# Performance work log

Hardware: AMD Instinct MI355X
Metric: run time of the kernel (lower is better)

## Reference

```python
import jax, jax.numpy as jnp
import numpy as np


def _tanh_approx(x):
    return x * jax.lax.rsqrt(1.0 + x * x)


def _lru(u, nu_log, gamma_log, Bm, Cm, Dv):
    # u: [B,T,H]; nu_log/gamma_log: [N]; Bm: [N,H]; Cm: [H,N]; Dv: [H]
    A = jnp.exp(-jnp.exp(nu_log))                       # [N], |A|<1
    Bu = jnp.exp(gamma_log) * jnp.einsum('bth,nh->btn', u, Bm)  # [B,T,N]
    A_full = jnp.broadcast_to(A, Bu.shape)
    # diagonal linear recurrence h_t = A*h_{t-1} + Bu_t via parallel scan
    def comb(c1, c2):
        a1, b1 = c1
        a2, b2 = c2
        return (a1 * a2, a2 * b1 + b2)
    _, h = jax.lax.associative_scan(comb, (A_full, Bu), axis=1)  # inclusive scan
    # module uses the state delayed by one step (out[0]=0, out[t]=h_{t-1})
    h_prev = jnp.pad(h[:, :-1, :], ((0, 0), (1, 0), (0, 0)))
    y = jnp.einsum('btn,hn->bth', h_prev, Cm) + Dv * u
    return y


def _model_block(x, nu_log, gamma_log, Bm, Cm, Dv, Wlin, blin):
    y = _lru(x, nu_log, gamma_log, Bm, Cm, Dv)
    y = _tanh_approx(y) @ Wlin.T + blin
    return y + x


def setup_inputs() -> dict:
    key = jax.random.key(0)
    ks = jax.random.split(key, 10)
    B_, T_, N, H, D = 16, 65536, 64, 64, 4
    r_min, r_max = 0.8, 1.0
    u = jax.random.uniform(ks[0], (D, N))
    nu_log = jnp.log(-0.5 * jnp.log(u * (r_max ** 2 - r_min ** 2) + r_min ** 2))
    A = jnp.exp(-jnp.exp(nu_log))
    gamma_log = jnp.log(jnp.sqrt(1.0 - A ** 2))
    Bm = jax.random.normal(ks[1], (D, N, H)) / np.sqrt(2.0 * H)
    Cm = jax.random.normal(ks[2], (D, H, N)) / np.sqrt(N)
    Dv = jax.random.normal(ks[3], (D, H))
    Wlin = jax.random.normal(ks[4], (D, H, H)) / np.sqrt(H)
    blin = jnp.zeros((D, H))
    Win = jax.random.normal(ks[5], (H, 1))
    Wout = jax.random.normal(ks[6], (1, H)) / np.sqrt(H)
    x = jax.random.normal(ks[7], (B_, T_, 1))
    return {"x": x, "Win": Win, "nu_log": nu_log, "gamma_log": gamma_log,
            "Bm": Bm, "Cm": Cm, "Dv": Dv, "Wlin": Wlin, "blin": blin, "Wout": Wout}


def reference(x, Win, nu_log, gamma_log, Bm, Cm, Dv, Wlin, blin, Wout):
    h = x @ Win.T  # [B,T,H]
    depth = nu_log.shape[0]
    for i in range(depth):
        h = _model_block(h, nu_log[i], gamma_log[i], Bm[i], Cm[i], Dv[i], Wlin[i], blin[i])
    return h @ Wout.T  # [B,T,1]
```

## Files before the change

### kernel.cpp

```cpp
#include <hip/hip_runtime.h>

#define B_ 16
#define T_ 65536
#define H_ 64
#define DEPTH_ 4
#define CHUNK 128
#define NCH (T_ / CHUNK)

typedef _Float16 f16;
typedef f16 f16x8 __attribute__((ext_vector_type(8)));
typedef float f32x4 __attribute__((ext_vector_type(4)));
typedef unsigned u32x4 __attribute__((ext_vector_type(4)));

#define MFMA(a, b, c) __builtin_amdgcn_mfma_f32_16x16x32_f16(a, b, c, 0, 0, 0)
#define SWZ(t, k) ((t) * 64 + ((k) ^ (((t) & 7) << 2)))

union U4F8 { u32x4 u; f16x8 h; };

__device__ __forceinline__ f16x8 ldfrag(const f16* p) { return *(const f16x8*)p; }

__global__ __launch_bounds__(256)
void prep(const float* __restrict__ Win, const float* __restrict__ nu,
          const float* __restrict__ ga, const float* __restrict__ Bm,
          const float* __restrict__ Cm, const float* __restrict__ Dv,
          const float* __restrict__ Wl,
          f16* __restrict__ BmH, f16* __restrict__ BmL,
          f16* __restrict__ CmH, f16* __restrict__ CmL,
          f16* __restrict__ WlH, float* __restrict__ atab, float* __restrict__ sc)
{
    const int tid = threadIdx.x;
    for (int l = 0; l < DEPTH_; ++l) {
        for (int idx = tid; idx < 4096; idx += 256) {
            int n = idx >> 6;
            float g = expf(ga[l * 64 + n]);
            float v = Bm[l * 4096 + idx] * g;
            f16 h = (f16)v;
            BmH[l * 4096 + idx] = h;
            BmL[l * 4096 + idx] = (f16)(v - (float)h);
            float cv = Cm[l * 4096 + idx];
            h = (f16)cv;
            CmH[l * 4096 + idx] = h;
            CmL[l * 4096 + idx] = (f16)(cv - (float)h);
            WlH[l * 4096 + idx] = (f16)Wl[l * 4096 + idx];
        }
        if (tid < 64) {
            int n = tid;
            float ex = expf(nu[l * 64 + n]);
            float a = expf(-ex);
            float g = expf(ga[l * 64 + n]);
            sc[l * 320 + n] = a;
            sc[l * 320 + 64 + n] = Dv[l * 64 + n];
            float bw = 0.f;
            for (int h2 = 0; h2 < 64; ++h2) bw += Bm[l * 4096 + n * 64 + h2] * Win[h2];
            sc[l * 320 + 128 + n] = bw * g;
            sc[l * 320 + 192 + n] = Dv[l * 64 + n] * Win[n];
            sc[l * 320 + 256 + n] = Win[n];
        }
        for (int idx = tid; idx < 8192; idx += 256) {
            int n = idx >> 7, j = idx & 127;
            float ex = expf(nu[l * 64 + n]);
            atab[l * 8192 + idx] = expf(-ex * (float)j);
        }
    }
}

__global__ __launch_bounds__(64)
void carry_x(const float* __restrict__ x, const float* __restrict__ sc0,
             float* __restrict__ carry)
{
    const int blk = blockIdx.x;
    const int b = blk >> 9, c = blk & (NCH - 1);
    const int n = threadIdx.x;
    const float a  = sc0[n];
    const float bw = sc0[128 + n];
    __shared__ float xs[64];
    const float* xp = x + (size_t)b * T_ + c * CHUNK;
    float s = 0.f;
    for (int bb = 0; bb < CHUNK / 64; ++bb) {
        __syncthreads();
        xs[n] = xp[bb * 64 + n];
        __syncthreads();
        #pragma unroll
        for (int tt = 0; tt < 64; ++tt) s = a * s + bw * xs[tt];
    }
    carry[((size_t)b * NCH + c) * 64 + n] = s;
}

__global__ __launch_bounds__(256)
void scan_carry(const float* __restrict__ nu_log, float* __restrict__ carry)
{
    const int b = blockIdx.x;
    const int tid = threadIdx.x;
    const int n = tid & 63, q = tid >> 6;
    const float ex = expf(nu_log[n]);
    const float aL = expf(-ex * (float)CHUNK);
    float* cp = carry + (size_t)b * NCH * 64 + n;
    __shared__ float part[4][64];

    const int SEG = NCH / 4;
    const int base = q * SEG;
    float p = 0.f;
    #pragma unroll 4
    for (int i = 0; i < SEG; ++i) {
        float v = cp[(size_t)(base + i) * 64];
        cp[(size_t)(base + i) * 64] = p;
        p = aL * p + v;
    }
    part[q][n] = p;
    __syncthreads();
    if (q > 0) {
        const float aLS = expf(-ex * (float)(CHUNK * SEG));
        float inc = 0.f;
        for (int qq = 0; qq < q; ++qq) inc = inc * aLS + part[qq][n];
        float qv = inc;
        #pragma unroll 4
        for (int i = 0; i < SEG; ++i) {
            cp[(size_t)(base + i) * 64] += qv;
            qv *= aL;
        }
    }
}

struct LPrep {
    const f16 *BmH, *BmL, *CmH, *CmL, *WlH;
    const float *av, *dvv, *bw, *dwin, *win;
    const f16 *BmHn, *BmLn;
    const float *atabn;
    const float *blin, *Wout;
};

template<int IN_X, int OUT_FINAL>
__global__ __launch_bounds__(256, 4)
void lru_fused(const float* __restrict__ x, f16* __restrict__ ubuf,
               LPrep P, float* __restrict__ carry, float* __restrict__ out)
{
    const int blk = blockIdx.x;
    const int b = blk >> 9, c = blk & (NCH - 1);
    const int t0 = c * CHUNK;
    const int tid = threadIdx.x;
    const int w = tid >> 6, lane = tid & 63;
    const int l15 = lane & 15, lq = lane >> 4;

    __shared__ float hpk[CHUNK * 64];
    __shared__ float swv[4][64];
    __shared__ float red[4][64];

    f16* ug = ubuf + ((size_t)b * T_ + t0) * 64;
    const float* xg = x + (size_t)b * T_ + t0;

    f16x8 ahu[2][2];
    if (!IN_X) {
        #pragma unroll
        for (int tt = 0; tt < 2; ++tt) {
            const f16* p = ug + (size_t)((2 * w + tt) * 16 + l15) * 64;
            U4F8 r0, r1;
            r0.u = __builtin_nontemporal_load((const u32x4*)(p + lq * 8));
            r1.u = __builtin_nontemporal_load((const u32x4*)(p + 32 + lq * 8));
            ahu[tt][0] = r0.h;
            ahu[tt][1] = r1.h;
        }
    }

    float av4[4];
    #pragma unroll
    for (int nt = 0; nt < 4; ++nt) av4[nt] = P.av[nt * 16 + l15];

    float xv[2][4];
    if (IN_X) {
        #pragma unroll
        for (int tt = 0; tt < 2; ++tt)
            #pragma unroll
            for (int r = 0; r < 4; ++r)
                xv[tt][r] = xg[32 * w + 16 * tt + 4 * lq + r];
    }

    f32x4 acc[4][2];
    if (IN_X) {
        #pragma unroll
        for (int nt = 0; nt < 4; ++nt) {
            float bwn = P.bw[nt * 16 + l15];
            #pragma unroll
            for (int tt = 0; tt < 2; ++tt)
                #pragma unroll
                for (int r = 0; r < 4; ++r) acc[nt][tt][r] = xv[tt][r] * bwn;
        }
    } else {
        #pragma unroll
        for (int nt = 0; nt < 4; ++nt) {
            int n = nt * 16 + l15;
            f16x8 bh0 = ldfrag(P.BmH + n * 64 + lq * 8);
            f16x8 bh1 = ldfrag(P.BmH + n * 64 + 32 + lq * 8);
            f16x8 bl0 = ldfrag(P.BmL + n * 64 + lq * 8);
            f16x8 bl1 = ldfrag(P.BmL + n * 64 + 32 + lq * 8);
            #pragma unroll
            for (int tt = 0; tt < 2; ++tt) {
                f32x4 a4v = {0.f, 0.f, 0.f, 0.f};
                a4v = MFMA(ahu[tt][0], bh0, a4v);
                a4v = MFMA(ahu[tt][0], bl0, a4v);
                a4v = MFMA(ahu[tt][1], bh1, a4v);
                a4v = MFMA(ahu[tt][1], bl1, a4v);
                acc[nt][tt] = a4v;
            }
        }
    }

    float Wb[4][2];
    #pragma unroll
    for (int nt = 0; nt < 4; ++nt) {
        float a = av4[nt], a2 = a * a, a4 = a2 * a2, a8 = a4 * a4, a16 = a8 * a8;
        float P0incl = 0.f;
        #pragma unroll
        for (int tt = 0; tt < 2; ++tt) {
            f32x4 xs = acc[nt][tt];
            float L0 = xs[0];
            float L1 = a * L0 + xs[1];
            float L2 = a * L1 + xs[2];
            float Cv = a * L2 + xs[3];
            float u1 = __shfl_up(Cv, 16);
            float t1 = Cv + ((lq >= 1) ? a4 * u1 : 0.f);
            float u2 = __shfl_up(t1, 32);
            float Pv = t1 + ((lq >= 2) ? a8 * u2 : 0.f);
            float E = __shfl_up(Pv, 16);
            E = (lq == 0) ? 0.f : E;
            if (tt == 0) { Wb[nt][0] = E; P0incl = Pv; }
            else {
                float B0 = __shfl(P0incl, 48 + l15);
                float a4lq = 1.f;
                if (lq & 1) a4lq *= a4;
                if (lq & 2) a4lq *= a8;
                Wb[nt][1] = E + a4lq * B0;
                if (lq == 3) swv[w][nt * 16 + l15] = Pv + a16 * B0;
            }
        }
    }
    __syncthreads();

    #pragma unroll
    for (int nt = 0; nt < 4; ++nt) {
        int n = nt * 16 + l15;
        float a = av4[nt], a2 = a * a, a4 = a2 * a2, a8 = a4 * a4, a16 = a8 * a8, a32 = a16 * a16;
        float inc = carry[((size_t)b * NCH + c) * 64 + n];
        for (int ww = 0; ww < w; ++ww) inc = inc * a32 + swv[ww][n];
        float a4lq = 1.f;
        if (lq & 1) a4lq *= a4;
        if (lq & 2) a4lq *= a8;
        #pragma unroll
        for (int tt = 0; tt < 2; ++tt) {
            float Z = Wb[nt][tt] + a4lq * (tt ? a16 : 1.f) * inc;
            float s = Z;
            #pragma unroll
            for (int r = 0; r < 4; ++r) {
                int t = 32 * w + 16 * tt + 4 * lq + r;
                hpk[SWZ(t, n)] = s;
                s = a * s + acc[nt][tt][r];
            }
        }
    }

    #pragma unroll
    for (int tt = 0; tt < 2; ++tt) {
        int tb = 2 * w + tt, trow = tb * 16 + l15, sw = (trow & 7) << 2;
        const float* hw = hpk + trow * 64;
        f16x8 ah[2], al[2];
        #pragma unroll
        for (int kk = 0; kk < 2; ++kk) {
            int kb = kk * 32 + lq * 8;
            float4 v0 = *(const float4*)(hw + (kb ^ sw));
            float4 v1 = *(const float4*)(hw + ((kb + 4) ^ sw));
            float vv[8] = {v0.x, v0.y, v0.z, v0.w, v1.x, v1.y, v1.z, v1.w};
            #pragma unroll
            for (int i = 0; i < 8; ++i) {
                f16 h = (f16)vv[i];
                ah[kk][i] = h;
                al[kk][i] = (f16)(vv[i] - (float)h);
            }
        }
        #pragma unroll
        for (int nt = 0; nt < 4; ++nt) {
            int n = nt * 16 + l15;
            f16x8 ch0 = ldfrag(P.CmH + n * 64 + lq * 8);
            f16x8 ch1 = ldfrag(P.CmH + n * 64 + 32 + lq * 8);
            f16x8 cl0 = ldfrag(P.CmL + n * 64 + lq * 8);
            f16x8 cl1 = ldfrag(P.CmL + n * 64 + 32 + lq * 8);
            f32x4 a4v = {0.f, 0.f, 0.f, 0.f};
            a4v = MFMA(ah[0], ch0, a4v);
            a4v = MFMA(al[0], ch0, a4v);
            a4v = MFMA(ah[0], cl0, a4v);
            a4v = MFMA(ah[1], ch1, a4v);
            a4v = MFMA(al[1], ch1, a4v);
            a4v = MFMA(ah[1], cl1, a4v);
            if (!IN_X) {
                float dv = P.dvv[n];
                f16 dh = (f16)dv, dl = (f16)(dv - (float)dh);
                f16x8 dfh, dfl;
                #pragma unroll
                for (int i2 = 0; i2 < 8; ++i2) { dfh[i2] = (f16)0.f; dfl[i2] = (f16)0.f; }
                int e = ((nt & 1) * 16 + l15) - lq * 8;
                if (e >= 0 && e < 8) { dfh[e] = dh; dfl[e] = dl; }
                a4v = MFMA(ahu[tt][nt >> 1], dfh, a4v);
                a4v = MFMA(ahu[tt][nt >> 1], dfl, a4v);
            }
            float dwin = IN_X ? P.dwin[n] : 0.f;
            #pragma unroll
            for (int r = 0; r < 4; ++r) {
                int t = tb * 16 + lq * 4 + r;
                float y = a4v[r];
                if (IN_X) y += xv[tt][r] * dwin;
                hpk[SWZ(t, n)] = y * rsqrtf(1.f + y * y);
            }
        }
    }

    f16* stg = (f16*)hpk;
    #pragma unroll
    for (int tt = 0; tt < 2; ++tt) {
        int tb = 2 * w + tt, trow = tb * 16 + l15, sw = (trow & 7) << 2;
        const float* hw = hpk + trow * 64;
        f16x8 t0f, t1f;
        #pragma unroll
        for (int kk = 0; kk < 2; ++kk) {
            int kb = kk * 32 + lq * 8;
            float4 v0 = *(const float4*)(hw + (kb ^ sw));
            float4 v1 = *(const float4*)(hw + ((kb + 4) ^ sw));
            float vv[8] = {v0.x, v0.y, v0.z, v0.w, v1.x, v1.y, v1.z, v1.w};
            #pragma unroll
            for (int i = 0; i < 8; ++i) {
                if (kk == 0) t0f[i] = (f16)vv[i]; else t1f[i] = (f16)vv[i];
            }
        }
        float val[4] = {0.f, 0.f, 0.f, 0.f};
        #pragma unroll
        for (int nt = 0; nt < 4; ++nt) {
            int n = nt * 16 + l15;
            f16x8 w0f = ldfrag(P.WlH + n * 64 + lq * 8);
            f16x8 w1f = ldfrag(P.WlH + n * 64 + 32 + lq * 8);
            f32x4 a4v = {0.f, 0.f, 0.f, 0.f};
            a4v = MFMA(t0f, w0f, a4v);
            a4v = MFMA(t1f, w1f, a4v);
            if (!IN_X) {
                f16x8 ifr;
                #pragma unroll
                for (int i2 = 0; i2 < 8; ++i2) ifr[i2] = (f16)0.f;
                int e = ((nt & 1) * 16 + l15) - lq * 8;
                if (e >= 0 && e < 8) ifr[e] = (f16)1.f;
                a4v = MFMA(ahu[tt][nt >> 1], ifr, a4v);
            }
            float blj = P.blin[n];
            float wij = IN_X ? P.win[n] : 0.f;
            float woj = OUT_FINAL ? P.Wout[n] : 0.f;
            #pragma unroll
            for (int r = 0; r < 4; ++r) {
                int t = tb * 16 + lq * 4 + r;
                float o = a4v[r] + blj;
                if (IN_X) o += xv[tt][r] * wij;
                if (OUT_FINAL) {
                    val[r] += o * woj;
                } else {
                    int g = n >> 1;
                    int word = t * 64 + (((g & ~3) ^ ((t & 7) << 2)) | (g & 3));
                    stg[word * 2 + (n & 1)] = (f16)o;
                }
            }
        }
        if (OUT_FINAL) {
            #pragma unroll
            for (int r = 0; r < 4; ++r) {
                float p = val[r];
                p += __shfl_xor(p, 1);
                p += __shfl_xor(p, 2);
                p += __shfl_xor(p, 4);
                p += __shfl_xor(p, 8);
                if (l15 == 0) out[(size_t)b * T_ + t0 + tb * 16 + lq * 4 + r] = p;
            }
        }
    }

    if (!OUT_FINAL) {
        #pragma unroll
        for (int i = 0; i < 4; ++i) {
            int row = 32 * w + i * 8 + (lane >> 3);
            int gg = 4 * (lane & 7);
            int word = row * 64 + (gg ^ ((row & 7) << 2));
            u32x4 cv = *(const u32x4*)(hpk + word);
            __builtin_nontemporal_store(cv, (u32x4*)(ug + (size_t)row * 64 + 8 * (lane & 7)));
        }

        float partial[4] = {0.f, 0.f, 0.f, 0.f};
        #pragma unroll
        for (int tt = 0; tt < 2; ++tt) {
            int tb = 2 * w + tt, arow = tb * 16 + l15, msk = (arow & 7) << 2;
            U4F8 av0, av1;
            av0.u = *(const u32x4*)(hpk + arow * 64 + ((4 * lq) ^ msk));
            av1.u = *(const u32x4*)(hpk + arow * 64 + ((16 + 4 * lq) ^ msk));
            #pragma unroll
            for (int nt = 0; nt < 4; ++nt) {
                int n = nt * 16 + l15;
                f16x8 bh0 = ldfrag(P.BmHn + n * 64 + lq * 8);
                f16x8 bh1 = ldfrag(P.BmHn + n * 64 + 32 + lq * 8);
                f16x8 bl0 = ldfrag(P.BmLn + n * 64 + lq * 8);
                f16x8 bl1 = ldfrag(P.BmLn + n * 64 + 32 + lq * 8);
                f32x4 a4v = {0.f, 0.f, 0.f, 0.f};
                a4v = MFMA(av0.h, bh0, a4v);
                a4v = MFMA(av0.h, bl0, a4v);
                a4v = MFMA(av1.h, bh1, a4v);
                a4v = MFMA(av1.h, bl1, a4v);
                float4 dp = *(const float4*)(P.atabn + n * 128 + 124 - tb * 16 - lq * 4);
                partial[nt] += a4v[0] * dp.w + a4v[1] * dp.z + a4v[2] * dp.y + a4v[3] * dp.x;
            }
        }
        #pragma unroll
        for (int nt = 0; nt < 4; ++nt) {
            float v = partial[nt];
            v += __shfl_xor(v, 16);
            v += __shfl_xor(v, 32);
            if (lq == 0) red[w][nt * 16 + l15] = v;
        }
        __syncthreads();
        if (w == 0)
            carry[((size_t)b * NCH + c) * 64 + lane] =
                red[0][lane] + red[1][lane] + red[2][lane] + red[3][lane];
    }
}

extern "C" void kernel_launch(void* const* d_in, const int* in_sizes, int n_in,
                              void* d_out, int out_size, void* d_ws, size_t ws_size,
                              hipStream_t stream)
{
    const float* x   = (const float*)d_in[0];
    const float* Win = (const float*)d_in[1];
    const float* nu  = (const float*)d_in[2];
    const float* ga  = (const float*)d_in[3];
    const float* Bm  = (const float*)d_in[4];
    const float* Cm  = (const float*)d_in[5];
    const float* Dv  = (const float*)d_in[6];
    const float* Wl  = (const float*)d_in[7];
    const float* bl  = (const float*)d_in[8];
    const float* Wo  = (const float*)d_in[9];
    float* out = (float*)d_out;

    char* p = (char*)d_ws;
    f16* ubuf = (f16*)p;            p += (size_t)B_ * T_ * 64 * sizeof(f16);
    float* carry = (float*)p;       p += (size_t)B_ * NCH * 64 * sizeof(float);
    f16* wBmH = (f16*)p;            p += 4 * 4096 * sizeof(f16);
    f16* wBmL = (f16*)p;            p += 4 * 4096 * sizeof(f16);
    f16* wCmH = (f16*)p;            p += 4 * 4096 * sizeof(f16);
    f16* wCmL = (f16*)p;            p += 4 * 4096 * sizeof(f16);
    f16* wWlH = (f16*)p;            p += 4 * 4096 * sizeof(f16);
    float* atab = (float*)p;        p += 4 * 8192 * sizeof(float);
    float* sc = (float*)p;          p += 4 * 320 * sizeof(float);

    dim3 grid(B_ * NCH), blk256(256), blk64(64), gscan(B_);

    prep<<<1, 256, 0, stream>>>(Win, nu, ga, Bm, Cm, Dv, Wl,
                                wBmH, wBmL, wCmH, wCmL, wWlH, atab, sc);
    carry_x<<<grid, blk64, 0, stream>>>(x, sc, carry);

    for (int l = 0; l < DEPTH_; ++l) {
        int ln = (l + 1 < DEPTH_) ? l + 1 : l;
        scan_carry<<<gscan, blk256, 0, stream>>>(nu + l * 64, carry);
        LPrep Pr;
        Pr.BmH = wBmH + l * 4096;  Pr.BmL = wBmL + l * 4096;
        Pr.CmH = wCmH + l * 4096;  Pr.CmL = wCmL + l * 4096;
        Pr.WlH = wWlH + l * 4096;
        Pr.av = sc + l * 320;       Pr.dvv = sc + l * 320 + 64;
        Pr.bw = sc + l * 320 + 128; Pr.dwin = sc + l * 320 + 192;
        Pr.win = sc + l * 320 + 256;
        Pr.BmHn = wBmH + ln * 4096; Pr.BmLn = wBmL + ln * 4096;
        Pr.atabn = atab + ln * 8192;
        Pr.blin = bl + l * 64; Pr.Wout = Wo;
        if (l == 0)
            lru_fused<1, 0><<<grid, blk256, 0, stream>>>(x, ubuf, Pr, carry, out);
        else if (l == DEPTH_ - 1)
            lru_fused<0, 1><<<grid, blk256, 0, stream>>>(x, ubuf, Pr, carry, out);
        else
            lru_fused<0, 0><<<grid, blk256, 0, stream>>>(x, ubuf, Pr, carry, out);
    }
}
```

Measured before the change: 1.410 ms.

## Free LDS for higher occupancy via global scratch, atomics and double-buffered carry

```diff
diff --git a/kernel.cpp b/kernel.cpp
--- a/kernel.cpp
+++ b/kernel.cpp
@@ -6,6 +6,7 @@
 #define DEPTH_ 4
 #define CHUNK 128
 #define NCH (T_ / CHUNK)
+#define NCH_LOG 9
 
 typedef _Float16 f16;
 typedef f16 f16x8 __attribute__((ext_vector_type(8)));
@@ -69,7 +70,7 @@
              float* __restrict__ carry)
 {
     const int blk = blockIdx.x;
-    const int b = blk >> 9, c = blk & (NCH - 1);
+    const int b = blk >> NCH_LOG, c = blk & (NCH - 1);
     const int n = threadIdx.x;
     const float a  = sc0[n];
     const float bw = sc0[128 + n];
@@ -87,7 +88,8 @@
 }
 
 __global__ __launch_bounds__(256)
-void scan_carry(const float* __restrict__ nu_log, float* __restrict__ carry)
+void scan_carry(const float* __restrict__ nu_log, float* __restrict__ carry,
+                float* __restrict__ carry_next)
 {
     const int b = blockIdx.x;
     const int tid = threadIdx.x;
@@ -95,6 +97,7 @@
     const float ex = expf(nu_log[n]);
     const float aL = expf(-ex * (float)CHUNK);
     float* cp = carry + (size_t)b * NCH * 64 + n;
+    float* zp = carry_next + (size_t)b * NCH * 64 + n;
     __shared__ float part[4][64];
 
     const int SEG = NCH / 4;
@@ -104,6 +107,7 @@
     for (int i = 0; i < SEG; ++i) {
         float v = cp[(size_t)(base + i) * 64];
         cp[(size_t)(base + i) * 64] = p;
+        zp[(size_t)(base + i) * 64] = 0.f;
         p = aL * p + v;
     }
     part[q][n] = p;
@@ -130,34 +134,32 @@
 };
 
 template<int IN_X, int OUT_FINAL>
-__global__ __launch_bounds__(256, 4)
+__global__ __launch_bounds__(256, 5)
 void lru_fused(const float* __restrict__ x, f16* __restrict__ ubuf,
-               LPrep P, float* __restrict__ carry, float* __restrict__ out)
+               LPrep P, const float* __restrict__ carry,
+               float* __restrict__ carry_out, float* __restrict__ swv_g,
+               float* __restrict__ out)
 {
     const int blk = blockIdx.x;
-    const int b = blk >> 9, c = blk & (NCH - 1);
+    const int b = blk >> NCH_LOG, c = blk & (NCH - 1);
     const int t0 = c * CHUNK;
     const int tid = threadIdx.x;
     const int w = tid >> 6, lane = tid & 63;
     const int l15 = lane & 15, lq = lane >> 4;
 
     __shared__ float hpk[CHUNK * 64];
-    __shared__ float swv[4][64];
-    __shared__ float red[4][64];
 
     f16* ug = ubuf + ((size_t)b * T_ + t0) * 64;
     const float* xg = x + (size_t)b * T_ + t0;
+    float* swvg = swv_g + (size_t)blk * 192;
 
     f16x8 ahu[2][2];
     if (!IN_X) {
         #pragma unroll
         for (int tt = 0; tt < 2; ++tt) {
             const f16* p = ug + (size_t)((2 * w + tt) * 16 + l15) * 64;
-            U4F8 r0, r1;
-            r0.u = __builtin_nontemporal_load((const u32x4*)(p + lq * 8));
-            r1.u = __builtin_nontemporal_load((const u32x4*)(p + 32 + lq * 8));
-            ahu[tt][0] = r0.h;
-            ahu[tt][1] = r1.h;
+            ahu[tt][0] = ldfrag(p + lq * 8);
+            ahu[tt][1] = ldfrag(p + 32 + lq * 8);
         }
     }
 
@@ -229,7 +231,8 @@
                 if (lq & 1) a4lq *= a4;
                 if (lq & 2) a4lq *= a8;
                 Wb[nt][1] = E + a4lq * B0;
-                if (lq == 3) swv[w][nt * 16 + l15] = Pv + a16 * B0;
+                if (lq == 3 && w < 3)
+                    swvg[w * 64 + nt * 16 + l15] = Pv + a16 * B0;
             }
         }
     }
@@ -239,8 +242,11 @@
     for (int nt = 0; nt < 4; ++nt) {
         int n = nt * 16 + l15;
         float a = av4[nt], a2 = a * a, a4 = a2 * a2, a8 = a4 * a4, a16 = a8 * a8, a32 = a16 * a16;
+        float s0 = swvg[n], s1 = swvg[64 + n], s2 = swvg[128 + n];
         float inc = carry[((size_t)b * NCH + c) * 64 + n];
-        for (int ww = 0; ww < w; ++ww) inc = inc * a32 + swv[ww][n];
+        if (w == 1)      inc = inc * a32 + s0;
+        else if (w == 2) inc = (inc * a32 + s0) * a32 + s1;
+        else if (w == 3) inc = ((inc * a32 + s0) * a32 + s1) * a32 + s2;
         float a4lq = 1.f;
         if (lq & 1) a4lq *= a4;
         if (lq & 2) a4lq *= a8;
@@ -289,23 +295,14 @@
             a4v = MFMA(ah[1], ch1, a4v);
             a4v = MFMA(al[1], ch1, a4v);
             a4v = MFMA(ah[1], cl1, a4v);
-            if (!IN_X) {
-                float dv = P.dvv[n];
-                f16 dh = (f16)dv, dl = (f16)(dv - (float)dh);
-                f16x8 dfh, dfl;
-                #pragma unroll
-                for (int i2 = 0; i2 < 8; ++i2) { dfh[i2] = (f16)0.f; dfl[i2] = (f16)0.f; }
-                int e = ((nt & 1) * 16 + l15) - lq * 8;
-                if (e >= 0 && e < 8) { dfh[e] = dh; dfl[e] = dl; }
-                a4v = MFMA(ahu[tt][nt >> 1], dfh, a4v);
-                a4v = MFMA(ahu[tt][nt >> 1], dfl, a4v);
-            }
             float dwin = IN_X ? P.dwin[n] : 0.f;
+            float dv   = IN_X ? 0.f : P.dvv[n];
             #pragma unroll
             for (int r = 0; r < 4; ++r) {
                 int t = tb * 16 + lq * 4 + r;
                 float y = a4v[r];
                 if (IN_X) y += xv[tt][r] * dwin;
+                else      y += dv * (float)ug[(size_t)t * 64 + n];
                 hpk[SWZ(t, n)] = y * rsqrtf(1.f + y * y);
             }
         }
@@ -337,14 +334,6 @@
             f32x4 a4v = {0.f, 0.f, 0.f, 0.f};
             a4v = MFMA(t0f, w0f, a4v);
             a4v = MFMA(t1f, w1f, a4v);
-            if (!IN_X) {
-                f16x8 ifr;
-                #pragma unroll
-                for (int i2 = 0; i2 < 8; ++i2) ifr[i2] = (f16)0.f;
-                int e = ((nt & 1) * 16 + l15) - lq * 8;
-                if (e >= 0 && e < 8) ifr[e] = (f16)1.f;
-                a4v = MFMA(ahu[tt][nt >> 1], ifr, a4v);
-            }
             float blj = P.blin[n];
             float wij = IN_X ? P.win[n] : 0.f;
             float woj = OUT_FINAL ? P.Wout[n] : 0.f;
@@ -353,6 +342,7 @@
                 int t = tb * 16 + lq * 4 + r;
                 float o = a4v[r] + blj;
                 if (IN_X) o += xv[tt][r] * wij;
+                else      o += (float)ug[(size_t)t * 64 + n];
                 if (OUT_FINAL) {
                     val[r] += o * woj;
                 } else {
@@ -382,7 +372,7 @@
             int gg = 4 * (lane & 7);
             int word = row * 64 + (gg ^ ((row & 7) << 2));
             u32x4 cv = *(const u32x4*)(hpk + word);
-            __builtin_nontemporal_store(cv, (u32x4*)(ug + (size_t)row * 64 + 8 * (lane & 7)));
+            *(u32x4*)(ug + (size_t)row * 64 + 8 * (lane & 7)) = cv;
         }
 
         float partial[4] = {0.f, 0.f, 0.f, 0.f};
@@ -413,12 +403,9 @@
             float v = partial[nt];
             v += __shfl_xor(v, 16);
             v += __shfl_xor(v, 32);
-            if (lq == 0) red[w][nt * 16 + l15] = v;
-        }
-        __syncthreads();
-        if (w == 0)
-            carry[((size_t)b * NCH + c) * 64 + lane] =
-                red[0][lane] + red[1][lane] + red[2][lane] + red[3][lane];
+            if (lq == 0)
+                atomicAdd(&carry_out[((size_t)b * NCH + c) * 64 + nt * 16 + l15], v);
+        }
     }
 }
 
@@ -440,7 +427,9 @@
 
     char* p = (char*)d_ws;
     f16* ubuf = (f16*)p;            p += (size_t)B_ * T_ * 64 * sizeof(f16);
-    float* carry = (float*)p;       p += (size_t)B_ * NCH * 64 * sizeof(float);
+    float* carryA = (float*)p;      p += (size_t)B_ * NCH * 64 * sizeof(float);
+    float* carryB = (float*)p;      p += (size_t)B_ * NCH * 64 * sizeof(float);
+    float* swvg = (float*)p;        p += (size_t)B_ * NCH * 192 * sizeof(float);
     f16* wBmH = (f16*)p;            p += 4 * 4096 * sizeof(f16);
     f16* wBmL = (f16*)p;            p += 4 * 4096 * sizeof(f16);
     f16* wCmH = (f16*)p;            p += 4 * 4096 * sizeof(f16);
@@ -451,13 +440,15 @@
 
     dim3 grid(B_ * NCH), blk256(256), blk64(64), gscan(B_);
 
-    prep<<<1, 256, 0, stream>>>(Win, nu, ga, Bm, Cm, Dv, Wl,
-                                wBmH, wBmL, wCmH, wCmL, wWlH, atab, sc);
-    carry_x<<<grid, blk64, 0, stream>>>(x, sc, carry);
-
+    prep<<<1, blk256, 0, stream>>>(Win, nu, ga, Bm, Cm, Dv, Wl,
+                                   wBmH, wBmL, wCmH, wCmL, wWlH, atab, sc);
+    carry_x<<<grid, blk64, 0, stream>>>(x, sc, carryA);
+
+    float* cR = carryA;
+    float* cW = carryB;
     for (int l = 0; l < DEPTH_; ++l) {
         int ln = (l + 1 < DEPTH_) ? l + 1 : l;
-        scan_carry<<<gscan, blk256, 0, stream>>>(nu + l * 64, carry);
+        scan_carry<<<gscan, blk256, 0, stream>>>(nu + l * 64, cR, cW);
         LPrep Pr;
         Pr.BmH = wBmH + l * 4096;  Pr.BmL = wBmL + l * 4096;
         Pr.CmH = wCmH + l * 4096;  Pr.CmL = wCmL + l * 4096;
@@ -469,10 +460,11 @@
         Pr.atabn = atab + ln * 8192;
         Pr.blin = bl + l * 64; Pr.Wout = Wo;
         if (l == 0)
-            lru_fused<1, 0><<<grid, blk256, 0, stream>>>(x, ubuf, Pr, carry, out);
+            lru_fused<1, 0><<<grid, blk256, 0, stream>>>(x, ubuf, Pr, cR, cW, swvg, out);
         else if (l == DEPTH_ - 1)
-            lru_fused<0, 1><<<grid, blk256, 0, stream>>>(x, ubuf, Pr, carry, out);
+            lru_fused<0, 1><<<grid, blk256, 0, stream>>>(x, ubuf, Pr, cR, cW, swvg, out);
         else
-            lru_fused<0, 0><<<grid, blk256, 0, stream>>>(x, ubuf, Pr, carry, out);
+            lru_fused<0, 0><<<grid, blk256, 0, stream>>>(x, ubuf, Pr, cR, cW, swvg, out);
+        float* tmp = cR; cR = cW; cW = tmp;
     }
 }
```

Result: slower. 1.539 ms (+9.1%).
